# Performance work log

Hardware: AMD Instinct MI355X
Metric: run time of the kernel (lower is better)

## Reference

```python
import jax, jax.numpy as jnp
import numpy as np

DIM = 128; D_STATE = 16; D_CONV = 4; EXPAND = 2
D_INNER = DIM * EXPAND            # 256
DT_RANK = (DIM + 15) // 16        # 8
B, H, W = 2, 56, 56


def _ln(x, w, b):
    m = jnp.mean(x, -1, keepdims=True)
    v = jnp.var(x, -1, keepdims=True)
    return (x - m) * jax.lax.rsqrt(v + 1e-5) * w + b


def _mamba(x, in_w, conv_w, conv_b, xproj_w, dt_w, dt_b, A_log, Dp, out_w):
    # x: (B, L, DIM)
    Bb, L, _ = x.shape
    xz = x @ in_w.T                                   # (B,L,2*D_INNER)
    xi, z = jnp.split(xz, 2, axis=-1)
    # causal depthwise conv1d (pad left d_conv-1, truncate to L)
    xc = jnp.transpose(xi, (0, 2, 1))                 # (B,D_INNER,L)
    xc = jax.lax.conv_general_dilated(
        xc, conv_w, (1,), [(D_CONV - 1, 0)],
        dimension_numbers=('NCH', 'OIH', 'NCH'),
        feature_group_count=D_INNER) + conv_b[None, :, None]
    xs = jax.nn.silu(jnp.transpose(xc, (0, 2, 1)))    # (B,L,D_INNER)
    dbl = xs @ xproj_w.T                              # (B,L,DT_RANK+2*D_STATE)
    dt = jax.nn.softplus(dbl[..., :DT_RANK] @ dt_w.T + dt_b)   # (B,L,D_INNER)
    Bc = dbl[..., DT_RANK:DT_RANK + D_STATE]          # (B,L,D_STATE)
    Cc = dbl[..., DT_RANK + D_STATE:]                 # (B,L,D_STATE)
    A = -jnp.exp(A_log)                               # (D_INNER,D_STATE)
    dA = jnp.exp(dt[..., None] * A)                   # (B,L,D_INNER,D_STATE)
    dBu = (dt * xs)[..., None] * Bc[:, :, None, :]    # (B,L,D_INNER,D_STATE)

    def step(h, inp):
        a, bu, c = inp
        h = a * h + bu                                # (B,D_INNER,D_STATE)
        return h, jnp.einsum('bdn,bn->bd', h, c)

    h0 = jnp.zeros((Bb, D_INNER, D_STATE), x.dtype)
    _, ys = jax.lax.scan(step, h0, (jnp.moveaxis(dA, 1, 0),
                                    jnp.moveaxis(dBu, 1, 0),
                                    jnp.moveaxis(Cc, 1, 0)))
    y = jnp.moveaxis(ys, 0, 1) + xs * Dp              # (B,L,D_INNER)
    y = y * jax.nn.silu(z)
    return y @ out_w.T                                # (B,L,DIM)


def _forward(x, norm_h_w, norm_h_b, norm_v_w, norm_v_b,
             dw_w, dw_b, pw_w, pw_b,
             h_in_w, h_conv_w, h_conv_b, h_xproj_w, h_dt_w, h_dt_b, h_A_log, h_D, h_out_w,
             v_in_w, v_conv_w, v_conv_b, v_xproj_w, v_dt_w, v_dt_b, v_A_log, v_D, v_out_w,
             ca_fc1_w, ca_fc2_w):
    Bb, C, Hh, Ww = x.shape
    # local branch: depthwise 3x3 + GELU + 1x1
    lf = jax.lax.conv_general_dilated(
        x, dw_w, (1, 1), [(1, 1), (1, 1)],
        dimension_numbers=('NCHW', 'OIHW', 'NCHW'),
        feature_group_count=C) + dw_b[None, :, None, None]
    lf = jax.nn.gelu(lf, approximate=False)
    lf = jnp.einsum('bchw,oc->bohw', lf, pw_w[:, :, 0, 0]) + pw_b[None, :, None, None]
    # horizontal scan: row-major tokens
    xh = _ln(x.reshape(Bb, C, Hh * Ww).transpose(0, 2, 1), norm_h_w, norm_h_b)
    oh = _mamba(xh, h_in_w, h_conv_w, h_conv_b, h_xproj_w, h_dt_w, h_dt_b,
                h_A_log, h_D, h_out_w)
    oh = oh.transpose(0, 2, 1).reshape(Bb, C, Hh, Ww)
    # vertical scan: column-major tokens
    xv = _ln(jnp.transpose(x, (0, 1, 3, 2)).reshape(Bb, C, Ww * Hh).transpose(0, 2, 1),
             norm_v_w, norm_v_b)
    ov = _mamba(xv, v_in_w, v_conv_w, v_conv_b, v_xproj_w, v_dt_w, v_dt_b,
                v_A_log, v_D, v_out_w)
    ov = jnp.transpose(ov.transpose(0, 2, 1).reshape(Bb, C, Ww, Hh), (0, 1, 3, 2))
    fused = oh + ov + lf
    # channel attention
    y = jnp.mean(fused, axis=(2, 3))                  # (B,C)
    y = jax.nn.sigmoid(jax.nn.relu(y @ ca_fc1_w.T) @ ca_fc2_w.T)
    return fused * y[:, :, None, None] + x


def setup_inputs() -> dict:
    key = jax.random.key(0)
    ks = iter(jax.random.split(key, 64))
    def nrm(shape, scale):
        return jax.random.normal(next(ks), shape, jnp.float32) * scale
    d = {}
    d['x'] = nrm((B, DIM, H, W), 1.0)
    d['norm_h_w'] = jnp.ones((DIM,), jnp.float32); d['norm_h_b'] = jnp.zeros((DIM,), jnp.float32)
    d['norm_v_w'] = jnp.ones((DIM,), jnp.float32); d['norm_v_b'] = jnp.zeros((DIM,), jnp.float32)
    d['dw_w'] = nrm((DIM, 1, 3, 3), 1.0 / 3.0)
    d['dw_b'] = jnp.zeros((DIM,), jnp.float32)
    d['pw_w'] = nrm((DIM, DIM, 1, 1), DIM ** -0.5)
    d['pw_b'] = jnp.zeros((DIM,), jnp.float32)
    for p in ('h', 'v'):
        d[p + '_in_w'] = nrm((2 * D_INNER, DIM), DIM ** -0.5)
        d[p + '_conv_w'] = nrm((D_INNER, 1, D_CONV), D_CONV ** -0.5)
        d[p + '_conv_b'] = jnp.zeros((D_INNER,), jnp.float32)
        d[p + '_xproj_w'] = nrm((DT_RANK + 2 * D_STATE, D_INNER), D_INNER ** -0.5)
        d[p + '_dt_w'] = nrm((D_INNER, DT_RANK), DT_RANK ** -0.5)
        d[p + '_dt_b'] = jnp.full((D_INNER,), -2.0, jnp.float32)  # small positive dt
        d[p + '_A_log'] = jnp.log(jnp.tile(jnp.arange(1, D_STATE + 1, dtype=jnp.float32), (D_INNER, 1)))
        d[p + '_D'] = jnp.ones((D_INNER,), jnp.float32)
        d[p + '_out_w'] = nrm((DIM, D_INNER), D_INNER ** -0.5)
    d['ca_fc1_w'] = nrm((DIM // 4, DIM), DIM ** -0.5)
    d['ca_fc2_w'] = nrm((DIM, DIM // 4), (DIM // 4) ** -0.5)
    return d


def reference(x, norm_h_w, norm_h_b, norm_v_w, norm_v_b,
              dw_w, dw_b, pw_w, pw_b,
              h_in_w, h_conv_w, h_conv_b, h_xproj_w, h_dt_w, h_dt_b, h_A_log, h_D, h_out_w,
              v_in_w, v_conv_w, v_conv_b, v_xproj_w, v_dt_w, v_dt_b, v_A_log, v_D, v_out_w,
              ca_fc1_w, ca_fc2_w):
    return _forward(x, norm_h_w, norm_h_b, norm_v_w, norm_v_b,
                    dw_w, dw_b, pw_w, pw_b,
                    h_in_w, h_conv_w, h_conv_b, h_xproj_w, h_dt_w, h_dt_b, h_A_log, h_D, h_out_w,
                    v_in_w, v_conv_w, v_conv_b, v_xproj_w, v_dt_w, v_dt_b, v_A_log, v_D, v_out_w,
                    ca_fc1_w, ca_fc2_w)
```

## Files before the change

### kernel.cpp

```cpp
#include <hip/hip_runtime.h>
#include <hip/hip_bf16.h>

typedef __hip_bfloat16 bf16;
__device__ __forceinline__ float b2f(bf16 v){ return __bfloat162float(v); }
__device__ __forceinline__ bf16 f2b(float v){ return __float2bfloat16(v); }

typedef __attribute__((ext_vector_type(8))) short frag_ab;
typedef __attribute__((ext_vector_type(4))) float frag_cd;
typedef __attribute__((ext_vector_type(4))) short short4v;

__device__ __forceinline__ frag_ab ld_frag_2xb64(const bf16* p){
  union { frag_ab f; short4v h[2]; } u;
  u.h[0] = *reinterpret_cast<const short4v*>(p);
  u.h[1] = *reinterpret_cast<const short4v*>(p+4);
  return u.f;
}

#define LLEN 3136
#define BATCH 2
#define NCHUNK 49
#define LC 64

__global__ void k_dwconv_gelu(const float* __restrict__ x, const float* __restrict__ dww,
                              const float* __restrict__ dwb, bf16* __restrict__ tmp,
                              float* __restrict__ YMEAN){
  int bc = blockIdx.x;
  int c = bc & 127;
  if (bc == 0 && blockIdx.y == 0 && threadIdx.x < 256) YMEAN[threadIdx.x] = 0.f;
  const float* xp = x + (size_t)bc*LLEN;
  float w[9];
  #pragma unroll
  for (int i=0;i<9;i++) w[i] = dww[c*9+i];
  float bias = dwb[c];
  int pstart = blockIdx.y * 784;
  int pend = pstart + 784;
  for (int p = pstart + threadIdx.x; p < pend; p += 256){
    int i = p/56, j = p%56;
    float acc = bias;
    #pragma unroll
    for (int a=0;a<3;a++){
      int ii = i + a - 1;
      if (ii < 0 || ii >= 56) continue;
      #pragma unroll
      for (int bb=0;bb<3;bb++){
        int jj = j + bb - 1;
        if (jj < 0 || jj >= 56) continue;
        acc += w[a*3+bb] * xp[ii*56+jj];
      }
    }
    float g = 0.5f*acc*(1.0f + erff(acc*0.70710678118654752f));
    tmp[(size_t)bc*LLEN + p] = f2b(g);
  }
}

__global__ void k_pw_gemm(const bf16* __restrict__ tmp, const float* __restrict__ pww,
                          const float* __restrict__ pwb, float* __restrict__ fused){
  int b  = blockIdx.z;
  int p0 = blockIdx.x * 64;
  int m0 = blockIdx.y * 64;
  const bf16* T = tmp + (size_t)b*128*LLEN;
  __shared__ __align__(16) bf16 sA[64][136];
  __shared__ __align__(16) bf16 sBt[64][132];
  int tid = threadIdx.x;
  #pragma unroll
  for (int r=0;r<8;r++){
    int idx = tid + r*256;
    int row = idx >> 5, c4 = (idx & 31)*4;
    float4 w4 = *reinterpret_cast<const float4*>(&pww[(size_t)(m0+row)*128 + c4]);
    bf16 t4[4] = {f2b(w4.x), f2b(w4.y), f2b(w4.z), f2b(w4.w)};
    *reinterpret_cast<double*>(&sA[row][c4]) = *reinterpret_cast<double*>(t4);
  }
  #pragma unroll
  for (int r=0;r<8;r++){
    int idx = tid + r*256;
    int c = idx >> 4, p4 = (idx & 15)*4;
    union { double d; bf16 v[4]; } u;
    u.d = *reinterpret_cast<const double*>(&T[(size_t)c*LLEN + p0 + p4]);
    #pragma unroll
    for (int j=0;j<4;j++) sBt[p4+j][c] = u.v[j];
  }
  __syncthreads();
  int wv2 = tid >> 6, lane = tid & 63;
  int qd = lane >> 4, mr = lane & 15;
  frag_cd acc[4] = {};
  #pragma unroll
  for (int k0=0;k0<128;k0+=32){
    frag_ab af = *reinterpret_cast<frag_ab*>(&sA[wv2*16+mr][k0+qd*8]);
    #pragma unroll
    for (int t=0;t<4;t++){
      frag_ab bfr = ld_frag_2xb64(&sBt[t*16+mr][k0+qd*8]);
      acc[t] = __builtin_amdgcn_mfma_f32_16x16x32_bf16(af, bfr, acc[t], 0, 0, 0);
    }
  }
  #pragma unroll
  for (int t=0;t<4;t++)
    #pragma unroll
    for (int r=0;r<4;r++){
      int m = m0 + wv2*16 + qd*4 + r;
      int p = p0 + t*16 + mr;
      fused[((size_t)b*128 + m)*LLEN + p] = acc[t][r] + pwb[m];
    }
}

__global__ void k_ln(const float* __restrict__ x, const float* nhw_, const float* nhb_,
                     const float* nvw_, const float* nvb_, bf16* __restrict__ xln){
  __shared__ float sx[128][57];
  __shared__ float smean[56], srstd[56];
  __shared__ float wh[128], bh[128], wv_[128], bv_[128];
  int h = blockIdx.x; int b = blockIdx.y;
  int tid = threadIdx.x;
  if (tid < 128){ wh[tid]=nhw_[tid]; bh[tid]=nhb_[tid];
                  wv_[tid]=nvw_[tid]; bv_[tid]=nvb_[tid]; }
  for (int idx = tid; idx < 128*56; idx += 256){
    int c = idx / 56, w = idx % 56;
    sx[c][w] = x[((size_t)(b*128+c))*LLEN + h*56 + w];
  }
  __syncthreads();
  if (tid < 56){
    float s=0.f, s2=0.f;
    for (int c=0;c<128;c++){ float v = sx[c][tid]; s+=v; s2+=v*v; }
    float m = s*(1.f/128.f);
    float var = s2*(1.f/128.f) - m*m;
    smean[tid]=m; srstd[tid]=rsqrtf(var+1e-5f);
  }
  __syncthreads();
  bf16* outh = xln;
  bf16* outv = xln + (size_t)BATCH*LLEN*128;
  for (int idx = tid; idx < 56*128; idx += 256){
    int w = idx >> 7, c = idx & 127;
    float v = (sx[c][w]-smean[w])*srstd[w];
    outh[((size_t)b*LLEN + h*56 + w)*128 + c] = f2b(v*wh[c]+bh[c]);
    outv[((size_t)b*LLEN + w*56 + h)*128 + c] = f2b(v*wv_[c]+bv_[c]);
  }
}

__global__ void k_inproj(const bf16* __restrict__ xln, const float* __restrict__ hw,
                         const float* __restrict__ vw, bf16* __restrict__ XI, bf16* __restrict__ Z){
  int dir = blockIdx.z;
  const bf16* A = xln + (size_t)dir*BATCH*LLEN*128;
  const float* W = dir ? vw : hw;
  int m0 = blockIdx.x*64, n0 = blockIdx.y*64;
  __shared__ __align__(16) bf16 sA[64][136];
  __shared__ __align__(16) bf16 sW[64][136];
  int tid = threadIdx.x;
  #pragma unroll
  for (int r=0;r<4;r++){
    int idx = tid + r*256;
    int row = idx >> 4, c8 = (idx & 15)*8;
    *reinterpret_cast<float4*>(&sA[row][c8]) =
        *reinterpret_cast<const float4*>(&A[(size_t)(m0+row)*128 + c8]);
  }
  #pragma unroll
  for (int r=0;r<8;r++){
    int idx = tid + r*256;
    int row = idx >> 5, c4 = (idx & 31)*4;
    float4 w4 = *reinterpret_cast<const float4*>(&W[(size_t)(n0+row)*128 + c4]);
    bf16 t4[4] = {f2b(w4.x), f2b(w4.y), f2b(w4.z), f2b(w4.w)};
    *reinterpret_cast<double*>(&sW[row][c4]) = *reinterpret_cast<double*>(t4);
  }
  __syncthreads();
  int wv2 = tid >> 6, lane = tid & 63;
  int qd = lane >> 4, mr = lane & 15;
  frag_cd acc[4] = {};
  #pragma unroll
  for (int k0=0;k0<128;k0+=32){
    frag_ab af = *reinterpret_cast<frag_ab*>(&sA[wv2*16+mr][k0+qd*8]);
    #pragma unroll
    for (int t=0;t<4;t++){
      frag_ab bfr = *reinterpret_cast<frag_ab*>(&sW[t*16+mr][k0+qd*8]);
      acc[t] = __builtin_amdgcn_mfma_f32_16x16x32_bf16(af, bfr, acc[t], 0, 0, 0);
    }
  }
  bf16* dst = (n0 < 256) ? XI : Z;
  int nb = n0 & 255;
  size_t dslab = (size_t)dir*BATCH*LLEN*256;
  #pragma unroll
  for (int t=0;t<4;t++)
    #pragma unroll
    for (int r=0;r<4;r++){
      int row = m0 + wv2*16 + qd*4 + r;
      int col = nb + t*16 + mr;
      dst[dslab + (size_t)row*256 + col] = f2b(acc[t][r]);
    }
}

__global__ void k_conv(const bf16* __restrict__ XI, const float* hw, const float* hb,
                       const float* vw, const float* vb, bf16* __restrict__ XS2){
  int dir = blockIdx.z;
  int b = blockIdx.y;
  int bd = dir*BATCH + b;
  int l0 = blockIdx.x * 32;
  const bf16* XId = XI + (size_t)bd*LLEN*256;
  const float* cw = dir ? vw : hw;
  const float* cb = dir ? vb : hb;
  __shared__ float sxi[35][256];
  int tid = threadIdx.x;
  for (int r = 0; r < 35; r++){
    int l = l0 - 3 + r;
    sxi[r][tid] = (l >= 0) ? b2f(XId[(size_t)l*256 + tid]) : 0.f;
  }
  __syncthreads();
  float w0=cw[tid*4], w1=cw[tid*4+1], w2=cw[tid*4+2], w3=cw[tid*4+3];
  float bias = cb[tid];
  size_t x2base = ((size_t)bd*16 + (tid>>4))*LLEN;
  int c16 = tid & 15;
  for (int ll=0; ll<32; ll++){
    float acc = bias + w0*sxi[ll][tid] + w1*sxi[ll+1][tid] + w2*sxi[ll+2][tid] + w3*sxi[ll+3][tid];
    float s = acc / (1.f + __expf(-acc));
    XS2[(x2base + l0 + ll)*16 + c16] = f2b(s);
  }
}

__global__ void k_dbl(const bf16* __restrict__ XS2, const float* __restrict__ hx,
                      const float* __restrict__ vx,
                      const float* hdw, const float* vdw, const float* hdb, const float* vdb,
                      const float* hA, const float* vA,
                      bf16* __restrict__ DT2, float* __restrict__ Bf, float* __restrict__ Cf,
                      float* __restrict__ Pbuf, float* __restrict__ Hbuf){
  int m0 = blockIdx.x*64;
  int bd = m0 / LLEN;
  int l0m = m0 % LLEN;
  int ck = l0m / LC;
  int dirq = bd >> 1;
  const float* W = dirq ? vx : hx;
  __shared__ __align__(16) bf16 sA[64][264];
  __shared__ __align__(16) bf16 sW[48][264];
  __shared__ float sdbl[64][49];
  int tid = threadIdx.x;
  #pragma unroll
  for (int r=0;r<8;r++){
    int idx = tid + r*256;
    int row = idx >> 5, c8 = (idx & 31)*8;
    size_t src = (((size_t)bd*16 + (c8>>4))*LLEN + l0m + row)*16 + (c8&15);
    *reinterpret_cast<float4*>(&sA[row][c8]) =
        *reinterpret_cast<const float4*>(&XS2[src]);
  }
  #pragma unroll
  for (int r=0;r<12;r++){
    int idx = tid + r*256;
    int row = idx >> 6, c4 = (idx & 63)*4;
    bf16 t4[4] = {f2b(0.f), f2b(0.f), f2b(0.f), f2b(0.f)};
    if (row < 40){
      float4 w4 = *reinterpret_cast<const float4*>(&W[(size_t)row*256 + c4]);
      t4[0]=f2b(w4.x); t4[1]=f2b(w4.y); t4[2]=f2b(w4.z); t4[3]=f2b(w4.w);
    }
    *reinterpret_cast<double*>(&sW[row][c4]) = *reinterpret_cast<double*>(t4);
  }
  __syncthreads();
  int wv2 = tid >> 6, lane = tid & 63;
  int qd = lane >> 4, mr = lane & 15;
  frag_cd acc[3] = {};
  #pragma unroll
  for (int k0=0;k0<256;k0+=32){
    frag_ab af = *reinterpret_cast<frag_ab*>(&sA[wv2*16+mr][k0+qd*8]);
    #pragma unroll
    for (int t=0;t<3;t++){
      frag_ab bfr = *reinterpret_cast<frag_ab*>(&sW[t*16+mr][k0+qd*8]);
      acc[t] = __builtin_amdgcn_mfma_f32_16x16x32_bf16(af, bfr, acc[t], 0, 0, 0);
    }
  }
  #pragma unroll
  for (int t=0;t<3;t++)
    #pragma unroll
    for (int r=0;r<4;r++){
      int col = t*16 + mr;
      if (col < 40) sdbl[wv2*16 + qd*4 + r][col] = acc[t][r];
    }
  __syncthreads();
  const float* dtw = dirq ? vdw : hdw;
  const float* dtb = dirq ? vdb : hdb;
  const float* Alog = dirq ? vA : hA;
  float w8[8];
  #pragma unroll
  for (int r=0;r<8;r++) w8[r] = dtw[tid*8+r];
  float biasv = dtb[tid];
  float Aq[16];
  #pragma unroll
  for (int n=0;n<16;n++) Aq[n] = -__expf(Alog[tid*16+n]);
  float hst[16] = {};
  float Pst[16];
  #pragma unroll
  for (int n=0;n<16;n++) Pst[n] = 1.f;
  size_t d2base = ((size_t)bd*16 + (tid>>4))*LLEN + l0m;
  int c16 = tid & 15;
  for (int row=0; row<64; row++){
    float a = biasv;
    #pragma unroll
    for (int r=0;r<8;r++) a += sdbl[row][r]*w8[r];
    float sv = (a > 20.f) ? a : __logf(1.f + __expf(a));
    bf16 svb16 = f2b(sv);
    DT2[(d2base + row)*16 + c16] = svb16;
    float svb = b2f(svb16);
    float u = b2f(sA[row][tid]);
    float au = svb*u;
    #pragma unroll
    for (int n=0;n<16;n++){
      float dA = __expf(svb * Aq[n]);
      hst[n] = dA*hst[n] + au*sdbl[row][8+n];
      Pst[n] *= dA;
    }
  }
  size_t pbase = (((size_t)bd*16 + (tid>>4))*NCHUNK + ck)*256 + (size_t)(tid&15)*16;
  #pragma unroll
  for (int n=0;n<16;n++){ Pbuf[pbase+n] = Pst[n]; Hbuf[pbase+n] = hst[n]; }
  #pragma unroll
  for (int r=0;r<8;r++){
    int idx = tid + r*256;
    int row = idx >> 5, o = idx & 31;
    float v = sdbl[row][8+o];
    size_t rr = (size_t)(m0+row)*16;
    if (o < 16) Bf[rr + o] = v;
    else        Cf[rr + (o-16)] = v;
  }
}

__global__ void k_scan2(const float* __restrict__ Pbuf, float* __restrict__ Hbuf){
  int q = blockIdx.x;
  int tid = threadIdx.x;
  float carry = 0.f;
  for (int k=0;k<NCHUNK;k++){
    size_t idx = ((size_t)q*NCHUNK + k)*256 + tid;
    float Pv = Pbuf[idx];
    float He = Hbuf[idx];
    Hbuf[idx] = carry;
    carry = Pv*carry + He;
  }
}

__global__ void k_scan3(const bf16* __restrict__ DT2, const bf16* __restrict__ XS2,
                        const float* __restrict__ Bc, const float* __restrict__ Cc,
                        const float* hA, const float* vA,
                        const float* __restrict__ Hbuf, bf16* __restrict__ ys){
  int bd = blockIdx.z;
  int g  = blockIdx.y;
  int ck = blockIdx.x;
  int l0 = ck*LC;
  const float* Bd = Bc + (size_t)bd*LLEN*16;
  const float* Cd = Cc + (size_t)bd*LLEN*16;
  bf16* yd = ys + (size_t)bd*LLEN*256;
  const float* Alog = (bd >> 1) ? vA : hA;
  int tid = threadIdx.x;
  int dl = tid >> 4, n = tid & 15;
  float A = -__expf(Alog[(g*16+dl)*16+n]);
  __shared__ float sdt[LC][16], sxs[LC][16], sB[LC][16], sC[LC][16];
  __shared__ __align__(16) float sp2[16][276];
  size_t base2 = (((size_t)bd*16 + g)*LLEN + l0)*16;
  #pragma unroll
  for (int r=0;r<4;r++){
    int idx = tid + r*256;
    sdt[idx>>4][idx&15] = b2f(DT2[base2 + idx]);
    sxs[idx>>4][idx&15] = b2f(XS2[base2 + idx]);
    (&sB[0][0])[idx] = Bd[(size_t)l0*16 + idx];
    (&sC[0][0])[idx] = Cd[(size_t)l0*16 + idx];
  }
  size_t sidx = (((size_t)bd*16 + g)*NCHUNK + ck)*256 + tid;
  float h = Hbuf[sidx];
  __syncthreads();
  int i_local = tid >> 4;
  int c16 = tid & 15;
  for (int i0=0; i0<LC; i0+=16){
    #pragma unroll
    for (int ii=0;ii<16;ii++){
      int i = i0 + ii;
      float a = sdt[i][dl];
      float u = sxs[i][dl];
      float dA = __expf(a * A);
      h = dA*h + (a*u)*sB[i][n];
      sp2[ii][tid] = h * sC[i][n];
    }
    __syncthreads();
    const float* row = &sp2[i_local][c16*16];
    float s = 0.f;
    #pragma unroll
    for (int k=0;k<4;k++){
      float4 v = *reinterpret_cast<const float4*>(row + k*4);
      s += v.x + v.y + v.z + v.w;
    }
    yd[(size_t)(l0+i0+i_local)*256 + g*16 + c16] = f2b(s);
    __syncthreads();
  }
}

__global__ void k_outgemm(const bf16* __restrict__ ys, const bf16* __restrict__ XS2,
                          const bf16* __restrict__ Z, const float* __restrict__ hD,
                          const float* __restrict__ vD, const float* __restrict__ how,
                          const float* __restrict__ vow, bf16* __restrict__ OD){
  int dir = blockIdx.z;
  size_t slab = (size_t)dir*BATCH*LLEN*256;
  const float* W = dir ? vow : how;
  const float* Dw = dir ? vD : hD;
  bf16* od = OD + (size_t)dir*BATCH*LLEN*128;
  int m0 = blockIdx.x*64, n0 = blockIdx.y*64;
  int bd = dir*2 + m0/LLEN;
  int lbase = m0 % LLEN;
  __shared__ __align__(16) bf16 sA[64][136];
  __shared__ __align__(16) bf16 sW[64][136];
  int tid = threadIdx.x;
  int wv2 = tid >> 6, lane = tid & 63;
  int qd = lane >> 4, mr = lane & 15;
  frag_cd acc[4] = {};
  for (int kc=0; kc<256; kc+=128){
    __syncthreads();
    #pragma unroll
    for (int r=0;r<4;r++){
      int idx = tid + r*256;
      int row = idx >> 4, c8 = (idx & 15)*8;
      int k = kc + c8;
      size_t e = slab + (size_t)(m0+row)*256 + k;
      size_t e2 = (((size_t)bd*16 + (k>>4))*LLEN + lbase + row)*16 + (k&15);
      bf16 yb[8], xb[8], zb[8], ob[8];
      *reinterpret_cast<float4*>(yb) = *reinterpret_cast<const float4*>(&ys[e]);
      *reinterpret_cast<float4*>(xb) = *reinterpret_cast<const float4*>(&XS2[e2]);
      *reinterpret_cast<float4*>(zb) = *reinterpret_cast<const float4*>(&Z[e]);
      #pragma unroll
      for (int j=0;j<8;j++){
        float Dv = Dw[k + j];
        float yv = b2f(yb[j]) + b2f(xb[j])*Dv;
        float zv = b2f(zb[j]);
        ob[j] = f2b(yv * (zv/(1.f+__expf(-zv))));
      }
      *reinterpret_cast<float4*>(&sA[row][c8]) = *reinterpret_cast<float4*>(ob);
    }
    #pragma unroll
    for (int r=0;r<8;r++){
      int idx = tid + r*256;
      int row = idx >> 5, c4 = (idx & 31)*4;
      float4 w4 = *reinterpret_cast<const float4*>(&W[(size_t)(n0+row)*256 + kc + c4]);
      bf16 t4[4] = {f2b(w4.x), f2b(w4.y), f2b(w4.z), f2b(w4.w)};
      *reinterpret_cast<double*>(&sW[row][c4]) = *reinterpret_cast<double*>(t4);
    }
    __syncthreads();
    #pragma unroll
    for (int k0=0;k0<128;k0+=32){
      frag_ab af = *reinterpret_cast<frag_ab*>(&sA[wv2*16+mr][k0+qd*8]);
      #pragma unroll
      for (int t=0;t<4;t++){
        frag_ab bfr = *reinterpret_cast<frag_ab*>(&sW[t*16+mr][k0+qd*8]);
        acc[t] = __builtin_amdgcn_mfma_f32_16x16x32_bf16(af, bfr, acc[t], 0, 0, 0);
      }
    }
  }
  #pragma unroll
  for (int t=0;t<4;t++)
    #pragma unroll
    for (int r=0;r<4;r++){
      int row = m0 + wv2*16 + qd*4 + r;
      int col = n0 + t*16 + mr;
      od[(size_t)row*128 + col] = f2b(acc[t][r]);
    }
}

__global__ void k_combine(const bf16* __restrict__ OD, float* __restrict__ fused,
                          float* __restrict__ YMEAN){
  int h = blockIdx.x;
  int b = blockIdx.y;
  __shared__ float sfu[56][129];
  int tid = threadIdx.x;
  const bf16* od0 = OD + (size_t)b*LLEN*128;
  const bf16* od1 = OD + (size_t)(BATCH + b)*LLEN*128;
  #pragma unroll 4
  for (int it=0; it<28; it++){
    int idx = it*256 + tid;
    int sp = idx >> 7, c = idx & 127;
    sfu[sp][c] = b2f(od0[(size_t)(h*56+sp)*128 + c]) + b2f(od1[(size_t)(sp*56+h)*128 + c]);
  }
  __syncthreads();
  int c = tid >> 1, half = tid & 1;
  float s = 0.f;
  size_t gbase = ((size_t)b*128 + c)*LLEN + h*56 + half*28;
  #pragma unroll
  for (int i=0;i<28;i++){
    float tot = fused[gbase+i] + sfu[half*28+i][c];
    fused[gbase+i] = tot;
    s += tot;
  }
  s += __shfl_xor(s, 1, 64);
  if (half == 0) atomicAdd(&YMEAN[b*128 + c], s);
}

__global__ void k_gate(const float* __restrict__ YMEAN, const float* fc1, const float* fc2,
                       float* __restrict__ gate){
  int b = blockIdx.x;
  __shared__ float ym[128], s1[32];
  int tid = threadIdx.x;
  ym[tid] = YMEAN[b*128 + tid] * (1.f/(float)LLEN);
  __syncthreads();
  if (tid < 32){
    float a = 0.f;
    for (int c=0;c<128;c++) a += ym[c]*fc1[tid*128+c];
    s1[tid] = fmaxf(a, 0.f);
  }
  __syncthreads();
  float a = 0.f;
  #pragma unroll
  for (int j=0;j<32;j++) a += s1[j]*fc2[tid*32+j];
  gate[b*128+tid] = 1.f/(1.f+__expf(-a));
}

__global__ void k_final(float* __restrict__ fused, const float* __restrict__ gate,
                        const float* __restrict__ x, float* __restrict__ out){
  int i = blockIdx.x*256 + threadIdx.x;
  if (i >= BATCH*128*LLEN) return;
  int bc = i / LLEN;
  float v = fused[i]*gate[bc] + x[i];
  out[i] = v;
}

extern "C" void kernel_launch(void* const* d_in, const int* in_sizes, int n_in,
                              void* d_out, int out_size, void* d_ws, size_t ws_size,
                              hipStream_t stream) {
  const float* x      = (const float*)d_in[0];
  const float* nhw    = (const float*)d_in[1];
  const float* nhb    = (const float*)d_in[2];
  const float* nvw    = (const float*)d_in[3];
  const float* nvb    = (const float*)d_in[4];
  const float* dww    = (const float*)d_in[5];
  const float* dwb    = (const float*)d_in[6];
  const float* pww    = (const float*)d_in[7];
  const float* pwb    = (const float*)d_in[8];
  const float* h_inw  = (const float*)d_in[9];
  const float* h_cw   = (const float*)d_in[10];
  const float* h_cb   = (const float*)d_in[11];
  const float* h_xw   = (const float*)d_in[12];
  const float* h_dtw  = (const float*)d_in[13];
  const float* h_dtb  = (const float*)d_in[14];
  const float* h_Al   = (const float*)d_in[15];
  const float* h_D    = (const float*)d_in[16];
  const float* h_ow   = (const float*)d_in[17];
  const float* v_inw  = (const float*)d_in[18];
  const float* v_cw   = (const float*)d_in[19];
  const float* v_cb   = (const float*)d_in[20];
  const float* v_xw   = (const float*)d_in[21];
  const float* v_dtw  = (const float*)d_in[22];
  const float* v_dtb  = (const float*)d_in[23];
  const float* v_Al   = (const float*)d_in[24];
  const float* v_D    = (const float*)d_in[25];
  const float* v_ow   = (const float*)d_in[26];
  const float* fc1    = (const float*)d_in[27];
  const float* fc2    = (const float*)d_in[28];

  float* FUSED = (float*)d_out;
  float* out   = (float*)d_out;

  char* base = (char*)d_ws;
  bf16*  TMP   = (bf16*)(base + 0);
  bf16*  XLN   = (bf16*)(base + 1605632);
  bf16*  DT2   = (bf16*)(base + 0);
  bf16*  OD    = (bf16*)(base + 0);
  bf16*  XI    = (bf16*)(base + 6422528);
  bf16*  YS    = (bf16*)(base + 6422528);
  float* Pbuf  = (float*)(base + 6422528);
  bf16*  Z     = (bf16*)(base + 12845056);
  bf16*  XS2   = (bf16*)(base + 19267584);
  float* Bf    = (float*)(base + 25690112);
  float* Cf    = (float*)(base + 26492928);
  float* Hbuf  = (float*)(base + 27295744);
  float* YMEAN = (float*)(base + 30507008);
  float* GATE  = (float*)(base + 30564352);

  k_dwconv_gelu<<<dim3(BATCH*128,4), dim3(256), 0, stream>>>(x, dww, dwb, TMP, YMEAN);
  k_pw_gemm<<<dim3(49,2,BATCH), dim3(256), 0, stream>>>(TMP, pww, pwb, FUSED);
  k_ln<<<dim3(56,BATCH), dim3(256), 0, stream>>>(x, nhw, nhb, nvw, nvb, XLN);
  k_inproj<<<dim3(98,8,2), dim3(256), 0, stream>>>(XLN, h_inw, v_inw, XI, Z);
  k_conv<<<dim3(98,BATCH,2), dim3(256), 0, stream>>>(XI, h_cw, h_cb, v_cw, v_cb, XS2);
  k_dbl<<<dim3(196), dim3(256), 0, stream>>>(XS2, h_xw, v_xw, h_dtw, v_dtw, h_dtb, v_dtb,
                                             h_Al, v_Al, DT2, Bf, Cf, Pbuf, Hbuf);
  k_scan2<<<dim3(64), dim3(256), 0, stream>>>(Pbuf, Hbuf);
  k_scan3<<<dim3(NCHUNK,16,4), dim3(256), 0, stream>>>(DT2, XS2, Bf, Cf, h_Al, v_Al, Hbuf, YS);
  k_outgemm<<<dim3(98,2,2), dim3(256), 0, stream>>>(YS, XS2, Z, h_D, v_D, h_ow, v_ow, OD);
  k_combine<<<dim3(56,BATCH), dim3(256), 0, stream>>>(OD, FUSED, YMEAN);
  k_gate<<<dim3(BATCH), dim3(128), 0, stream>>>(YMEAN, fc1, fc2, GATE);
  k_final<<<dim3((BATCH*128*LLEN+255)/256), dim3(256), 0, stream>>>(FUSED, GATE, x, out);
}
```

Baseline: 257.3 us.

## Fuse pointwise GEMM with branch combine and fold gate into final pass

The pointwise-conv GEMM is moved after the Mamba branches and merged with the combine step. Each tile adds the horizontal and transposed vertical outputs plus bias in registers and accumulates the channel means with shuffles and atomics. This drops one full read-modify-write of the fused buffer. The gate MLP is recomputed per block inside the final elementwise kernel, which removes two launches. TMP is moved to a workspace region that later kernels do not overwrite, and each final block now repeats a small fc1/fc2 computation.

After: 257.8 us. About the same (+0.2%).

```diff
diff --git a/kernel.cpp b/kernel.cpp
--- a/kernel.cpp
+++ b/kernel.cpp
@@ -51,55 +51,6 @@
     float g = 0.5f*acc*(1.0f + erff(acc*0.70710678118654752f));
     tmp[(size_t)bc*LLEN + p] = f2b(g);
   }
-}
-
-__global__ void k_pw_gemm(const bf16* __restrict__ tmp, const float* __restrict__ pww,
-                          const float* __restrict__ pwb, float* __restrict__ fused){
-  int b  = blockIdx.z;
-  int p0 = blockIdx.x * 64;
-  int m0 = blockIdx.y * 64;
-  const bf16* T = tmp + (size_t)b*128*LLEN;
-  __shared__ __align__(16) bf16 sA[64][136];
-  __shared__ __align__(16) bf16 sBt[64][132];
-  int tid = threadIdx.x;
-  #pragma unroll
-  for (int r=0;r<8;r++){
-    int idx = tid + r*256;
-    int row = idx >> 5, c4 = (idx & 31)*4;
-    float4 w4 = *reinterpret_cast<const float4*>(&pww[(size_t)(m0+row)*128 + c4]);
-    bf16 t4[4] = {f2b(w4.x), f2b(w4.y), f2b(w4.z), f2b(w4.w)};
-    *reinterpret_cast<double*>(&sA[row][c4]) = *reinterpret_cast<double*>(t4);
-  }
-  #pragma unroll
-  for (int r=0;r<8;r++){
-    int idx = tid + r*256;
-    int c = idx >> 4, p4 = (idx & 15)*4;
-    union { double d; bf16 v[4]; } u;
-    u.d = *reinterpret_cast<const double*>(&T[(size_t)c*LLEN + p0 + p4]);
-    #pragma unroll
-    for (int j=0;j<4;j++) sBt[p4+j][c] = u.v[j];
-  }
-  __syncthreads();
-  int wv2 = tid >> 6, lane = tid & 63;
-  int qd = lane >> 4, mr = lane & 15;
-  frag_cd acc[4] = {};
-  #pragma unroll
-  for (int k0=0;k0<128;k0+=32){
-    frag_ab af = *reinterpret_cast<frag_ab*>(&sA[wv2*16+mr][k0+qd*8]);
-    #pragma unroll
-    for (int t=0;t<4;t++){
-      frag_ab bfr = ld_frag_2xb64(&sBt[t*16+mr][k0+qd*8]);
-      acc[t] = __builtin_amdgcn_mfma_f32_16x16x32_bf16(af, bfr, acc[t], 0, 0, 0);
-    }
-  }
-  #pragma unroll
-  for (int t=0;t<4;t++)
-    #pragma unroll
-    for (int r=0;r<4;r++){
-      int m = m0 + wv2*16 + qd*4 + r;
-      int p = p0 + t*16 + mr;
-      fused[((size_t)b*128 + m)*LLEN + p] = acc[t][r] + pwb[m];
-    }
 }
 
 __global__ void k_ln(const float* __restrict__ x, const float* nhw_, const float* nhb_,
@@ -450,60 +401,111 @@
     }
 }
 
-__global__ void k_combine(const bf16* __restrict__ OD, float* __restrict__ fused,
-                          float* __restrict__ YMEAN){
-  int h = blockIdx.x;
-  int b = blockIdx.y;
-  __shared__ float sfu[56][129];
-  int tid = threadIdx.x;
+__global__ void k_pwcomb(const bf16* __restrict__ tmp, const float* __restrict__ pww,
+                         const float* __restrict__ pwb, const bf16* __restrict__ OD,
+                         float* __restrict__ fused, float* __restrict__ YMEAN){
+  int p0 = blockIdx.x * 64;
+  int m0 = blockIdx.y * 64;
+  int b  = blockIdx.z;
+  const bf16* T = tmp + (size_t)b*128*LLEN;
   const bf16* od0 = OD + (size_t)b*LLEN*128;
   const bf16* od1 = OD + (size_t)(BATCH + b)*LLEN*128;
-  #pragma unroll 4
-  for (int it=0; it<28; it++){
-    int idx = it*256 + tid;
-    int sp = idx >> 7, c = idx & 127;
-    sfu[sp][c] = b2f(od0[(size_t)(h*56+sp)*128 + c]) + b2f(od1[(size_t)(sp*56+h)*128 + c]);
-  }
-  __syncthreads();
-  int c = tid >> 1, half = tid & 1;
-  float s = 0.f;
-  size_t gbase = ((size_t)b*128 + c)*LLEN + h*56 + half*28;
-  #pragma unroll
-  for (int i=0;i<28;i++){
-    float tot = fused[gbase+i] + sfu[half*28+i][c];
-    fused[gbase+i] = tot;
-    s += tot;
-  }
-  s += __shfl_xor(s, 1, 64);
-  if (half == 0) atomicAdd(&YMEAN[b*128 + c], s);
-}
-
-__global__ void k_gate(const float* __restrict__ YMEAN, const float* fc1, const float* fc2,
-                       float* __restrict__ gate){
-  int b = blockIdx.x;
+  __shared__ __align__(16) bf16 sA[64][136];
+  __shared__ __align__(16) bf16 sBt[64][132];
+  __shared__ float sOD[64][65];
+  int tid = threadIdx.x;
+  #pragma unroll
+  for (int r=0;r<8;r++){
+    int idx = tid + r*256;
+    int row = idx >> 5, c4 = (idx & 31)*4;
+    float4 w4 = *reinterpret_cast<const float4*>(&pww[(size_t)(m0+row)*128 + c4]);
+    bf16 t4[4] = {f2b(w4.x), f2b(w4.y), f2b(w4.z), f2b(w4.w)};
+    *reinterpret_cast<double*>(&sA[row][c4]) = *reinterpret_cast<double*>(t4);
+  }
+  #pragma unroll
+  for (int r=0;r<8;r++){
+    int idx = tid + r*256;
+    int c = idx >> 4, p4 = (idx & 15)*4;
+    union { double d; bf16 v[4]; } u;
+    u.d = *reinterpret_cast<const double*>(&T[(size_t)c*LLEN + p0 + p4]);
+    #pragma unroll
+    for (int j=0;j<4;j++) sBt[p4+j][c] = u.v[j];
+  }
+  #pragma unroll
+  for (int r=0;r<8;r++){
+    int idx = tid + r*256;
+    int prow = idx >> 5, mp = (idx & 31)*2;
+    int p = p0 + prow;
+    int pi = p/56, pj = p%56;
+    int pt = pj*56 + pi;
+    bf16 a0[2], a1[2];
+    *reinterpret_cast<float*>(a0) = *reinterpret_cast<const float*>(&od0[(size_t)p*128 + m0 + mp]);
+    *reinterpret_cast<float*>(a1) = *reinterpret_cast<const float*>(&od1[(size_t)pt*128 + m0 + mp]);
+    sOD[prow][mp]   = b2f(a0[0]) + b2f(a1[0]);
+    sOD[prow][mp+1] = b2f(a0[1]) + b2f(a1[1]);
+  }
+  __syncthreads();
+  int wv2 = tid >> 6, lane = tid & 63;
+  int qd = lane >> 4, mr = lane & 15;
+  frag_cd acc[4] = {};
+  #pragma unroll
+  for (int k0=0;k0<128;k0+=32){
+    frag_ab af = *reinterpret_cast<frag_ab*>(&sA[wv2*16+mr][k0+qd*8]);
+    #pragma unroll
+    for (int t=0;t<4;t++){
+      frag_ab bfr = ld_frag_2xb64(&sBt[t*16+mr][k0+qd*8]);
+      acc[t] = __builtin_amdgcn_mfma_f32_16x16x32_bf16(af, bfr, acc[t], 0, 0, 0);
+    }
+  }
+  #pragma unroll
+  for (int r=0;r<4;r++){
+    int m = m0 + wv2*16 + qd*4 + r;
+    float bias = pwb[m];
+    float s = 0.f;
+    #pragma unroll
+    for (int t=0;t<4;t++){
+      int p = p0 + t*16 + mr;
+      float val = acc[t][r] + bias + sOD[t*16+mr][m - m0];
+      fused[((size_t)b*128 + m)*LLEN + p] = val;
+      s += val;
+    }
+    s += __shfl_xor(s, 1, 16);
+    s += __shfl_xor(s, 2, 16);
+    s += __shfl_xor(s, 4, 16);
+    s += __shfl_xor(s, 8, 16);
+    if (mr == 0) atomicAdd(&YMEAN[b*128 + m], s);
+  }
+}
+
+__global__ void k_final_gate(const float* __restrict__ fused, const float* __restrict__ YMEAN,
+                             const float* __restrict__ fc1, const float* __restrict__ fc2,
+                             const float* __restrict__ x, float* __restrict__ out){
+  int bc = blockIdx.y;
+  int b = bc >> 7, c = bc & 127;
   __shared__ float ym[128], s1[32];
-  int tid = threadIdx.x;
-  ym[tid] = YMEAN[b*128 + tid] * (1.f/(float)LLEN);
+  __shared__ float gsh;
+  int tid = threadIdx.x;
+  if (tid < 128) ym[tid] = YMEAN[b*128 + tid] * (1.f/(float)LLEN);
   __syncthreads();
   if (tid < 32){
     float a = 0.f;
-    for (int c=0;c<128;c++) a += ym[c]*fc1[tid*128+c];
+    for (int cc=0;cc<128;cc++) a += ym[cc]*fc1[tid*128+cc];
     s1[tid] = fmaxf(a, 0.f);
   }
   __syncthreads();
-  float a = 0.f;
-  #pragma unroll
-  for (int j=0;j<32;j++) a += s1[j]*fc2[tid*32+j];
-  gate[b*128+tid] = 1.f/(1.f+__expf(-a));
-}
-
-__global__ void k_final(float* __restrict__ fused, const float* __restrict__ gate,
-                        const float* __restrict__ x, float* __restrict__ out){
-  int i = blockIdx.x*256 + threadIdx.x;
-  if (i >= BATCH*128*LLEN) return;
-  int bc = i / LLEN;
-  float v = fused[i]*gate[bc] + x[i];
-  out[i] = v;
+  if (tid == 0){
+    float a = 0.f;
+    #pragma unroll
+    for (int j=0;j<32;j++) a += s1[j]*fc2[c*32+j];
+    gsh = 1.f/(1.f+__expf(-a));
+  }
+  __syncthreads();
+  float g = gsh;
+  int p = blockIdx.x*256 + tid;
+  if (p < LLEN){
+    size_t i = (size_t)bc*LLEN + p;
+    out[i] = fused[i]*g + x[i];
+  }
 }
 
 extern "C" void kernel_launch(void* const* d_in, const int* in_sizes, int n_in,
@@ -543,7 +545,6 @@
   float* out   = (float*)d_out;
 
   char* base = (char*)d_ws;
-  bf16*  TMP   = (bf16*)(base + 0);
   bf16*  XLN   = (bf16*)(base + 1605632);
   bf16*  DT2   = (bf16*)(base + 0);
   bf16*  OD    = (bf16*)(base + 0);
@@ -556,10 +557,9 @@
   float* Cf    = (float*)(base + 26492928);
   float* Hbuf  = (float*)(base + 27295744);
   float* YMEAN = (float*)(base + 30507008);
-  float* GATE  = (float*)(base + 30564352);
+  bf16*  TMP   = (bf16*)(base + 30508032);
 
   k_dwconv_gelu<<<dim3(BATCH*128,4), dim3(256), 0, stream>>>(x, dww, dwb, TMP, YMEAN);
-  k_pw_gemm<<<dim3(49,2,BATCH), dim3(256), 0, stream>>>(TMP, pww, pwb, FUSED);
   k_ln<<<dim3(56,BATCH), dim3(256), 0, stream>>>(x, nhw, nhb, nvw, nvb, XLN);
   k_inproj<<<dim3(98,8,2), dim3(256), 0, stream>>>(XLN, h_inw, v_inw, XI, Z);
   k_conv<<<dim3(98,BATCH,2), dim3(256), 0, stream>>>(XI, h_cw, h_cb, v_cw, v_cb, XS2);
@@ -568,7 +568,6 @@
   k_scan2<<<dim3(64), dim3(256), 0, stream>>>(Pbuf, Hbuf);
   k_scan3<<<dim3(NCHUNK,16,4), dim3(256), 0, stream>>>(DT2, XS2, Bf, Cf, h_Al, v_Al, Hbuf, YS);
   k_outgemm<<<dim3(98,2,2), dim3(256), 0, stream>>>(YS, XS2, Z, h_D, v_D, h_ow, v_ow, OD);
-  k_combine<<<dim3(56,BATCH), dim3(256), 0, stream>>>(OD, FUSED, YMEAN);
-  k_gate<<<dim3(BATCH), dim3(128), 0, stream>>>(YMEAN, fc1, fc2, GATE);
-  k_final<<<dim3((BATCH*128*LLEN+255)/256), dim3(256), 0, stream>>>(FUSED, GATE, x, out);
-}
+  k_pwcomb<<<dim3(49,2,BATCH), dim3(256), 0, stream>>>(TMP, pww, pwb, OD, FUSED, YMEAN);
+  k_final_gate<<<dim3(13,256), dim3(256), 0, stream>>>(FUSED, YMEAN, fc1, fc2, x, out);
+}
```
